# Performance work log

Measured on AMD Instinct MI355X. Metric: run time of the kernel, lower is better.

## Reference

```python
import jax, jax.numpy as jnp
import numpy as np

KH, KW, PAD = 3, 3, 1
K = KH * KW


def _offset_conv(x, w, b):
    # standard 3x3 conv, stride 1, padding 1, NCHW
    out = jax.lax.conv_general_dilated(
        x, w, window_strides=(1, 1), padding=((PAD, PAD), (PAD, PAD)),
        dimension_numbers=("NCHW", "OIHW", "NCHW"))
    return out + b[None, :, None, None]


def _deform_conv(x, offsets, weight, groups):
    # torchvision.ops.deform_conv2d semantics: offset channels are
    # (dy, dx) pairs per kernel tap; zero padding outside the image;
    # bilinear interpolation with per-corner validity masks.
    B, C, H, W = x.shape
    off = offsets.reshape(B, K, 2, H, W)
    dy, dx = off[:, :, 0], off[:, :, 1]                      # [B,K,H,W]

    ky, kx = jnp.meshgrid(jnp.arange(KH), jnp.arange(KW), indexing="ij")
    ky = ky.reshape(K); kx = kx.reshape(K)
    base_y = (jnp.arange(H)[None, :, None] + (ky - PAD)[:, None, None])  # [K,H,1]
    base_x = (jnp.arange(W)[None, None, :] + (kx - PAD)[:, None, None])  # [K,1,W]
    py = base_y[None].astype(x.dtype) + dy                   # [B,K,H,W]
    px = base_x[None].astype(x.dtype) + dx

    # torchvision returns 0 when the sample point is fully outside
    valid = (py > -1) & (py < H) & (px > -1) & (px < W)
    y0 = jnp.floor(py); x0 = jnp.floor(px)
    ly = py - y0; lx = px - x0                               # fractional parts
    y0i = y0.astype(jnp.int32); x0i = x0.astype(jnp.int32)

    def gather(yi, xi):
        ok = (yi >= 0) & (yi < H) & (xi >= 0) & (xi < W) & valid
        yic = jnp.clip(yi, 0, H - 1)
        xic = jnp.clip(xi, 0, W - 1)
        def per_b(img, yb, xb, okb):
            # img [C,H,W]; yb,xb,okb [K,H,W] -> [C,K,H,W]
            return img[:, yb, xb] * okb[None].astype(img.dtype)
        return jax.vmap(per_b)(x, yic, xic, ok)

    v00 = gather(y0i, x0i)
    v01 = gather(y0i, x0i + 1)
    v10 = gather(y0i + 1, x0i)
    v11 = gather(y0i + 1, x0i + 1)
    w00 = ((1 - ly) * (1 - lx))[:, None]
    w01 = ((1 - ly) * lx)[:, None]
    w10 = (ly * (1 - lx))[:, None]
    w11 = (ly * lx)[:, None]
    sampled = v00 * w00 + v01 * w01 + v10 * w10 + v11 * w11  # [B,C,K,H,W]

    Cg = C // groups
    sampled = sampled.reshape(B, groups, Cg, K, H, W)
    wg = weight.reshape(groups, Cg, Cg, K)                   # [G, Cout_g, Cin_g, K]
    out = jnp.einsum("bgckhw,gock->bgohw", sampled, wg)
    return out.reshape(B, C, H, W)


def setup_inputs() -> dict:
    key = jax.random.key(0)
    k1, k2, k3, k4 = jax.random.split(key, 4)
    B, C, H, W, groups = 4, 256, 96, 96, 4
    x = jax.random.normal(k1, (B, C, H, W), dtype=jnp.float32)
    # small offset-conv weights keep learned offsets in a realistic range
    offset_w = jax.random.normal(k2, (2 * K, C, KH, KW), dtype=jnp.float32) * 0.02
    offset_b = jax.random.normal(k3, (2 * K,), dtype=jnp.float32) * 0.1
    fan_in = (C // groups) * KH * KW
    weight = jax.random.normal(k4, (C, C // groups, KH, KW), dtype=jnp.float32) / np.sqrt(fan_in)
    return {"x": x, "offset_w": offset_w, "offset_b": offset_b,
            "weight": weight, "groups": groups}


def reference(x, offset_w, offset_b, weight, groups):
    offsets = _offset_conv(x, offset_w, offset_b)
    return _deform_conv(x, offsets, weight, groups)
```

## Files before the change

### kernel.cpp

```cpp
#include <hip/hip_runtime.h>
#include <hip/hip_bf16.h>
#include <math.h>

#define B_   4
#define C_   256
#define H_   96
#define W_   96
#define HW_  (H_ * W_)
#define G_   4
#define CG_  64
#define K_   9
#define PW_  98
#define PROW_ (PW_ * C_)

typedef __bf16  bf16x8 __attribute__((ext_vector_type(8)));
typedef float   f32x4  __attribute__((ext_vector_type(4)));

__global__ __launch_bounds__(256) void transpose_prep_kernel(
    const float* __restrict__ x, const float* __restrict__ ow,
    const float* __restrict__ wt, __hip_bfloat16* __restrict__ xtp,
    __hip_bfloat16* __restrict__ aOW, __hip_bfloat16* __restrict__ aW)
{
    int t = threadIdx.x;
    int gid = blockIdx.x * 256 + t;

    if (gid < 73728) {
        int j    = gid & 7;
        int r    = gid >> 3;
        int lane = r & 63;  r >>= 6;
        int mt   = r & 1;   r >>= 1;
        int ks   = r & 7;   r >>= 3;
        int tap  = r;
        int m = mt * 16 + (lane & 15);
        int c = ks * 32 + (lane >> 4) * 8 + j;
        float v = (m < 18) ? ow[(m * 256 + c) * 9 + tap] : 0.f;
        aOW[gid] = __float2bfloat16(v);
    }
    if (gid < 147456) {
        int j    = gid & 7;
        int r    = gid >> 3;
        int lane = r & 63;  r >>= 6;
        int ct   = r & 1;   r >>= 1;
        int half = r & 1;   r >>= 1;
        int ks   = r & 1;   r >>= 1;
        int tap  = r % 9;
        int g    = r / 9;
        int c  = ks * 32 + (lane >> 4) * 8 + j;
        int co = half * 32 + ct * 16 + (lane & 15);
        float v = wt[(((g * CG_ + co) * CG_ + c) * 9) + tap];
        aW[gid] = __float2bfloat16(v);
    }

    int blk = blockIdx.x;
    int ch  = blk & 1;
    int bh  = blk >> 1;
    int b = bh / H_, h = bh - b * H_;
    __shared__ __align__(16) __hip_bfloat16 tile[96 * 136];
    const float* xb = x + (size_t)b * C_ * HW_ + (size_t)(ch * 128) * HW_ + h * W_;
#pragma unroll
    for (int r = 0; r < 12; ++r) {
        int e4 = r * 256 + t;
        int c = e4 / 24, w4 = e4 - c * 24;
        float4 v = *(const float4*)(xb + (size_t)c * HW_ + w4 * 4);
        int base = (w4 * 4) * 136 + c;
        tile[base      ] = __float2bfloat16(v.x);
        tile[base + 136] = __float2bfloat16(v.y);
        tile[base + 272] = __float2bfloat16(v.z);
        tile[base + 408] = __float2bfloat16(v.w);
    }
    __syncthreads();
    __hip_bfloat16* ob = xtp + ((size_t)(b * PW_ + h + 1) * PW_ + 1) * C_ + ch * 128;
#pragma unroll
    for (int i = 0; i < 6; ++i) {
        int sIdx = i * 256 + t;
        int px = sIdx >> 4, seg = sIdx & 15;
        *(bf16x8*)(ob + px * 256 + seg * 8) =
            *(const bf16x8*)(&tile[px * 136 + seg * 8]);
    }
    bf16x8 z = {};
    if (t < 32) {
        int side = t >> 4, i = t & 15;
        *(bf16x8*)(xtp + ((size_t)(b * PW_ + h + 1) * PW_ + side * 97) * C_
                   + ch * 128 + i * 8) = z;
    }
    if (h == 0 || h == 95) {
        int row = (h == 0) ? 0 : 97;
        __hip_bfloat16* rb = xtp + (size_t)(b * PW_ + row) * PROW_;
        for (int i = 0; i < 7; ++i) {
            int idx = i * 256 + t;
            if (idx < 1568) *(bf16x8*)(rb + (ch * 1568 + idx) * 8) = z;
        }
    }
}

__global__ __launch_bounds__(384) void offset_conv_kernel(
    const __hip_bfloat16* __restrict__ xtp, const __hip_bfloat16* __restrict__ aOW,
    const float* __restrict__ bias, __hip_bfloat16* __restrict__ off2)
{
    int blk = blockIdx.x;
    int xcd = blk & 7;
    int s   = blk >> 3;
    int unit = xcd * 96 + s;
    int bh   = unit >> 1;
    int whalf = unit & 1;
    int b   = bh / H_, h = bh % H_;
    int t = threadIdx.x, lane = t & 63;
    int ww = __builtin_amdgcn_readfirstlane(t >> 6);
    int nt = ww % 3;
    int kh = ww / 3;
    int w0 = whalf * 48 + nt * 16;
    int ml = lane & 15, kq = lane >> 4;

    __shared__ __align__(16) __hip_bfloat16 aS[2][8192];
    __shared__ __align__(16) f32x4 red[3 * 64 * 2];

    auto stage = [&](int tap, int p) {
        const bf16x8* src = (const bf16x8*)(aOW + tap * 8192);
        bf16x8* dst = (bf16x8*)aS[p];
        for (int i = t; i < 1024; i += 384) dst[i] = src[i];
    };

    f32x4 acc0 = {}, acc1 = {};
    const __hip_bfloat16* xb = xtp + (size_t)b * (PW_ * PROW_);

    stage(0, 0);
    __syncthreads();
    for (int tap = 0; tap < 9; ++tap) {
        if (tap < 8) stage(tap + 1, (tap + 1) & 1);
        int ky = tap / 3, kx = tap - ky * 3;
        const __hip_bfloat16* brow =
            xb + ((h + ky) * PW_ + (w0 + ml + kx)) * C_ + kh * 128 + kq * 8;
        const __hip_bfloat16* arow = aS[tap & 1] + kh * 4096 + lane * 8;
#pragma unroll
        for (int ks = 0; ks < 4; ++ks) {
            bf16x8 bf = *(const bf16x8*)(brow + ks * 32);
            bf16x8 a0 = *(const bf16x8*)(arow + ks * 1024);
            bf16x8 a1 = *(const bf16x8*)(arow + ks * 1024 + 512);
            acc0 = __builtin_amdgcn_mfma_f32_16x16x32_bf16(a0, bf, acc0, 0, 0, 0);
            acc1 = __builtin_amdgcn_mfma_f32_16x16x32_bf16(a1, bf, acc1, 0, 0, 0);
        }
        __syncthreads();
    }

    if (kh == 1) {
        red[(nt * 64 + lane) * 2 + 0] = acc0;
        red[(nt * 64 + lane) * 2 + 1] = acc1;
    }
    __syncthreads();
    if (kh == 0) {
        acc0 += red[(nt * 64 + lane) * 2 + 0];
        acc1 += red[(nt * 64 + lane) * 2 + 1];
        int w = w0 + ml;
#pragma unroll
        for (int r = 0; r < 4; ++r) {
            int j0 = kq * 4 + r;
            off2[((size_t)(b * 9 + (j0 >> 1)) * HW_ + h * W_ + w) * 2 + (j0 & 1)] =
                __float2bfloat16(acc0[r] + bias[j0]);
            int j1 = 16 + kq * 4 + r;
            if (j1 < 18)
                off2[((size_t)(b * 9 + (j1 >> 1)) * HW_ + h * W_ + w) * 2 + (j1 & 1)] =
                    __float2bfloat16(acc1[r] + bias[j1]);
        }
    }
}

__global__ __launch_bounds__(384, 4) void deform_kernel(
    const __hip_bfloat16* __restrict__ xtp, const __hip_bfloat16* __restrict__ off2,
    const __hip_bfloat16* __restrict__ aW, float* __restrict__ out)
{
    int blk = blockIdx.x;
    int xcd = blk & 7;
    int s   = blk >> 3;
    int bg  = xcd * 2 + (s / H_);
    int h   = s % H_;
    int g   = bg & 3;
    int b   = bg >> 2;
    int t    = threadIdx.x;
    int lane = t & 63;
    int wave = __builtin_amdgcn_readfirstlane(t >> 6);
    int half   = wave & 1;
    int wthird = wave >> 1;

    __shared__ __align__(16) __hip_bfloat16 sS[2][96 * 72];

    const __hip_bfloat16* xb =
        xtp + ((size_t)b * (PW_ * PW_) + PW_ + 1) * C_ + g * CG_;
    const __hip_bfloat162* offp =
        (const __hip_bfloat162*)off2 + (size_t)(b * 9) * HW_ + h * W_;
    const __hip_bfloat16* aWg = aW + (g * 9) * 4096;

    int tw8 = t >> 3;
    int j8  = (t & 7) * 8;

    f32x4 acc[2][2] = {};

    auto sample = [&](int k, int p) {
        int ky = k / 3, kx = k - ky * 3;
#pragma unroll
        for (int it = 0; it < 2; ++it) {
            int w  = it * 48 + tw8;
            __hip_bfloat162 pr = offp[k * HW_ + w];
            float py = (float)(h + ky - 1) + __bfloat162float(pr.x);
            float px = (float)(w + kx - 1) + __bfloat162float(pr.y);
            bool valid = (py > -1.f) && (py < (float)H_) &&
                         (px > -1.f) && (px < (float)W_);
            float y0f = floorf(py), x0f = floorf(px);
            float ly = py - y0f, lx = px - x0f;
            int y0 = (int)y0f, x0 = (int)x0f;
            int base = valid ? (y0 * PW_ + x0) * C_ : -(PW_ + 1) * C_;
            float wy1 = valid ? ly : 0.f;
            float wy0 = valid ? (1.f - ly) : 0.f;
            float mx0 = 1.f - lx;
            float bw00 = wy0 * mx0, bw01 = wy0 * lx;
            float bw10 = wy1 * mx0, bw11 = wy1 * lx;
            const __hip_bfloat16* p0 = xb + base + j8;
            bf16x8 c00 = *(const bf16x8*)(p0);
            bf16x8 c01 = *(const bf16x8*)(p0 + C_);
            bf16x8 c10 = *(const bf16x8*)(p0 + PROW_);
            bf16x8 c11 = *(const bf16x8*)(p0 + PROW_ + C_);
            bf16x8 r;
#pragma unroll
            for (int e = 0; e < 8; ++e) {
                float v = bw00 * (float)c00[e] + bw01 * (float)c01[e]
                        + bw10 * (float)c10[e] + bw11 * (float)c11[e];
                r[e] = (__bf16)v;
            }
            *(bf16x8*)(&sS[p][w * 72 + j8]) = r;
        }
    };

    auto mmtap = [&](int k, int p) {
        bf16x8 afrag[2][2];
        const __hip_bfloat16* at = aWg + k * 4096 + half * 1024 + lane * 8;
#pragma unroll
        for (int ks = 0; ks < 2; ++ks)
#pragma unroll
            for (int ct = 0; ct < 2; ++ct)
                afrag[ks][ct] = *(const bf16x8*)(at + ks * 2048 + ct * 512);
#pragma unroll
        for (int ks = 0; ks < 2; ++ks) {
#pragma unroll
            for (int wt = 0; wt < 2; ++wt) {
                int wrow = wthird * 32 + wt * 16 + (lane & 15);
                bf16x8 bfrag = *(const bf16x8*)(
                    &sS[p][wrow * 72 + ks * 32 + (lane >> 4) * 8]);
                acc[0][wt] = __builtin_amdgcn_mfma_f32_16x16x32_bf16(
                                 afrag[ks][0], bfrag, acc[0][wt], 0, 0, 0);
                acc[1][wt] = __builtin_amdgcn_mfma_f32_16x16x32_bf16(
                                 afrag[ks][1], bfrag, acc[1][wt], 0, 0, 0);
            }
        }
    };

    sample(0, 0);
    __syncthreads();
    for (int k = 0; k < K_; ++k) {
        if (k < K_ - 1) sample(k + 1, (k + 1) & 1);
        mmtap(k, k & 1);
        __syncthreads();
    }

    float* ob = out + ((b * C_ + g * CG_ + half * 32) * HW_) + h * W_ + wthird * 32;
    int rbase = (lane >> 4) * 4;
    int ncol  = lane & 15;
#pragma unroll
    for (int ct = 0; ct < 2; ++ct)
#pragma unroll
        for (int wt = 0; wt < 2; ++wt)
#pragma unroll
            for (int r = 0; r < 4; ++r)
                __builtin_nontemporal_store(
                    acc[ct][wt][r],
                    ob + (ct * 16 + rbase + r) * HW_ + wt * 16 + ncol);
}

extern "C" void kernel_launch(void* const* d_in, const int* in_sizes, int n_in,
                              void* d_out, int out_size, void* d_ws, size_t ws_size,
                              hipStream_t stream) {
    const float* x    = (const float*)d_in[0];
    const float* ow   = (const float*)d_in[1];
    const float* obi  = (const float*)d_in[2];
    const float* wt   = (const float*)d_in[3];

    __hip_bfloat16* xtp  = (__hip_bfloat16*)d_ws;
    __hip_bfloat16* off2 = xtp + (size_t)B_ * PW_ * PW_ * C_;
    __hip_bfloat16* aW   = off2 + (size_t)B_ * 9 * HW_ * 2;
    __hip_bfloat16* aOW  = aW + 147456;

    transpose_prep_kernel<<<B_ * H_ * 2, 256, 0, stream>>>(x, ow, wt, xtp, aOW, aW);
    offset_conv_kernel<<<B_ * H_ * 2, 384, 0, stream>>>(xtp, aOW, obi, off2);
    deform_kernel<<<B_ * G_ * H_, 384, 0, stream>>>(xtp, off2, aW, (float*)d_out);
}
```

Measured before the change: 169.4 us.

## Split deform kernel blocks into half-row tiles for more parallelism

Each deform block now processes 48 output columns instead of a full 96-wide row, doubling the grid to 3072 blocks and halving shared memory and accumulator registers. Each thread samples one pixel per tap instead of two, and each wave does half as many MFMAs per tap. The final barrier after the last tap is dropped. More blocks improve occupancy and latency hiding, but the weight fragments from global memory are now reloaded by twice as many blocks, and each block does less work between barriers.

```diff
diff --git a/kernel.cpp b/kernel.cpp
--- a/kernel.cpp
+++ b/kernel.cpp
@@ -170,85 +170,77 @@
 {
     int blk = blockIdx.x;
     int xcd = blk & 7;
-    int s   = blk >> 3;
-    int bg  = xcd * 2 + (s / H_);
-    int h   = s % H_;
+    int u   = blk >> 3;
+    int wh  = u & 1;
+    int ru  = u >> 1;
+    int bg  = xcd * 2 + (ru / H_);
+    int h   = ru % H_;
     int g   = bg & 3;
     int b   = bg >> 2;
     int t    = threadIdx.x;
     int lane = t & 63;
     int wave = __builtin_amdgcn_readfirstlane(t >> 6);
-    int half   = wave & 1;
-    int wthird = wave >> 1;
-
-    __shared__ __align__(16) __hip_bfloat16 sS[2][96 * 72];
+    int half = wave & 1;
+    int wt3  = wave >> 1;
+
+    __shared__ __align__(16) __hip_bfloat16 sS[2][48 * 72];
 
     const __hip_bfloat16* xb =
         xtp + ((size_t)b * (PW_ * PW_) + PW_ + 1) * C_ + g * CG_;
     const __hip_bfloat162* offp =
-        (const __hip_bfloat162*)off2 + (size_t)(b * 9) * HW_ + h * W_;
+        (const __hip_bfloat162*)off2 + (size_t)(b * 9) * HW_ + h * W_ + wh * 48;
     const __hip_bfloat16* aWg = aW + (g * 9) * 4096;
 
-    int tw8 = t >> 3;
-    int j8  = (t & 7) * 8;
-
-    f32x4 acc[2][2] = {};
+    int tw = t >> 3;
+    int j8 = (t & 7) * 8;
+    int w  = wh * 48 + tw;
+
+    f32x4 acc[2] = {};
 
     auto sample = [&](int k, int p) {
         int ky = k / 3, kx = k - ky * 3;
-#pragma unroll
-        for (int it = 0; it < 2; ++it) {
-            int w  = it * 48 + tw8;
-            __hip_bfloat162 pr = offp[k * HW_ + w];
-            float py = (float)(h + ky - 1) + __bfloat162float(pr.x);
-            float px = (float)(w + kx - 1) + __bfloat162float(pr.y);
-            bool valid = (py > -1.f) && (py < (float)H_) &&
-                         (px > -1.f) && (px < (float)W_);
-            float y0f = floorf(py), x0f = floorf(px);
-            float ly = py - y0f, lx = px - x0f;
-            int y0 = (int)y0f, x0 = (int)x0f;
-            int base = valid ? (y0 * PW_ + x0) * C_ : -(PW_ + 1) * C_;
-            float wy1 = valid ? ly : 0.f;
-            float wy0 = valid ? (1.f - ly) : 0.f;
-            float mx0 = 1.f - lx;
-            float bw00 = wy0 * mx0, bw01 = wy0 * lx;
-            float bw10 = wy1 * mx0, bw11 = wy1 * lx;
-            const __hip_bfloat16* p0 = xb + base + j8;
-            bf16x8 c00 = *(const bf16x8*)(p0);
-            bf16x8 c01 = *(const bf16x8*)(p0 + C_);
-            bf16x8 c10 = *(const bf16x8*)(p0 + PROW_);
-            bf16x8 c11 = *(const bf16x8*)(p0 + PROW_ + C_);
-            bf16x8 r;
-#pragma unroll
-            for (int e = 0; e < 8; ++e) {
-                float v = bw00 * (float)c00[e] + bw01 * (float)c01[e]
-                        + bw10 * (float)c10[e] + bw11 * (float)c11[e];
-                r[e] = (__bf16)v;
-            }
-            *(bf16x8*)(&sS[p][w * 72 + j8]) = r;
-        }
+        __hip_bfloat162 pr = offp[k * HW_ + tw];
+        float py = (float)(h + ky - 1) + __bfloat162float(pr.x);
+        float px = (float)(w + kx - 1) + __bfloat162float(pr.y);
+        bool valid = (py > -1.f) && (py < (float)H_) &&
+                     (px > -1.f) && (px < (float)W_);
+        float y0f = floorf(py), x0f = floorf(px);
+        float ly = py - y0f, lx = px - x0f;
+        int y0 = (int)y0f, x0 = (int)x0f;
+        int base = valid ? (y0 * PW_ + x0) * C_ : -(PW_ + 1) * C_;
+        float wy1 = valid ? ly : 0.f;
+        float wy0 = valid ? (1.f - ly) : 0.f;
+        float mx0 = 1.f - lx;
+        float bw00 = wy0 * mx0, bw01 = wy0 * lx;
+        float bw10 = wy1 * mx0, bw11 = wy1 * lx;
+        const __hip_bfloat16* p0 = xb + base + j8;
+        bf16x8 c00 = *(const bf16x8*)(p0);
+        bf16x8 c01 = *(const bf16x8*)(p0 + C_);
+        bf16x8 c10 = *(const bf16x8*)(p0 + PROW_);
+        bf16x8 c11 = *(const bf16x8*)(p0 + PROW_ + C_);
+        bf16x8 r;
+#pragma unroll
+        for (int e = 0; e < 8; ++e) {
+            float v = bw00 * (float)c00[e] + bw01 * (float)c01[e]
+                    + bw10 * (float)c10[e] + bw11 * (float)c11[e];
+            r[e] = (__bf16)v;
+        }
+        *(bf16x8*)(&sS[p][tw * 72 + j8]) = r;
     };
 
     auto mmtap = [&](int k, int p) {
-        bf16x8 afrag[2][2];
         const __hip_bfloat16* at = aWg + k * 4096 + half * 1024 + lane * 8;
-#pragma unroll
-        for (int ks = 0; ks < 2; ++ks)
-#pragma unroll
-            for (int ct = 0; ct < 2; ++ct)
-                afrag[ks][ct] = *(const bf16x8*)(at + ks * 2048 + ct * 512);
+        int wrow = wt3 * 16 + (lane & 15);
 #pragma unroll
         for (int ks = 0; ks < 2; ++ks) {
-#pragma unroll
-            for (int wt = 0; wt < 2; ++wt) {
-                int wrow = wthird * 32 + wt * 16 + (lane & 15);
-                bf16x8 bfrag = *(const bf16x8*)(
-                    &sS[p][wrow * 72 + ks * 32 + (lane >> 4) * 8]);
-                acc[0][wt] = __builtin_amdgcn_mfma_f32_16x16x32_bf16(
-                                 afrag[ks][0], bfrag, acc[0][wt], 0, 0, 0);
-                acc[1][wt] = __builtin_amdgcn_mfma_f32_16x16x32_bf16(
-                                 afrag[ks][1], bfrag, acc[1][wt], 0, 0, 0);
-            }
+            bf16x8 a0 = *(const bf16x8*)(at + ks * 2048);
+            bf16x8 a1 = *(const bf16x8*)(at + ks * 2048 + 512);
+            bf16x8 bfrag = *(const bf16x8*)(
+                &sS[p][wrow * 72 + ks * 32 + (lane >> 4) * 8]);
+            acc[0] = __builtin_amdgcn_mfma_f32_16x16x32_bf16(
+                         a0, bfrag, acc[0], 0, 0, 0);
+            acc[1] = __builtin_amdgcn_mfma_f32_16x16x32_bf16(
+                         a1, bfrag, acc[1], 0, 0, 0);
         }
     };
 
@@ -257,21 +249,19 @@
     for (int k = 0; k < K_; ++k) {
         if (k < K_ - 1) sample(k + 1, (k + 1) & 1);
         mmtap(k, k & 1);
-        __syncthreads();
-    }
-
-    float* ob = out + ((b * C_ + g * CG_ + half * 32) * HW_) + h * W_ + wthird * 32;
+        if (k < K_ - 1) __syncthreads();
+    }
+
+    float* ob = out + ((b * C_ + g * CG_ + half * 32) * HW_)
+              + h * W_ + wh * 48 + wt3 * 16;
     int rbase = (lane >> 4) * 4;
     int ncol  = lane & 15;
 #pragma unroll
     for (int ct = 0; ct < 2; ++ct)
 #pragma unroll
-        for (int wt = 0; wt < 2; ++wt)
-#pragma unroll
-            for (int r = 0; r < 4; ++r)
-                __builtin_nontemporal_store(
-                    acc[ct][wt][r],
-                    ob + (ct * 16 + rbase + r) * HW_ + wt * 16 + ncol);
+        for (int r = 0; r < 4; ++r)
+            __builtin_nontemporal_store(
+                acc[ct][r], ob + (ct * 16 + rbase + r) * HW_ + ncol);
 }
 
 extern "C" void kernel_launch(void* const* d_in, const int* in_sizes, int n_in,
@@ -289,5 +279,5 @@
 
     transpose_prep_kernel<<<B_ * H_ * 2, 256, 0, stream>>>(x, ow, wt, xtp, aOW, aW);
     offset_conv_kernel<<<B_ * H_ * 2, 384, 0, stream>>>(xtp, aOW, obi, off2);
-    deform_kernel<<<B_ * G_ * H_, 384, 0, stream>>>(xtp, off2, aW, (float*)d_out);
-}
+    deform_kernel<<<B_ * G_ * H_ * 2, 384, 0, stream>>>(xtp, off2, aW, (float*)d_out);
+}
```

Measured after the change: 170.8 us. Within noise of the previous version (+0.8%).
